# Kernel tuning notes

Hardware: AMD Instinct MI355X
Metric: run time of the kernel (lower is better)

Reference implementation:

```python
import jax, jax.numpy as jnp
import numpy as np

KERNEL_SIZE = 32
STRIDE = 16
SELECT_SIZE = 64
TOP_N = 16
NUM_INIT = 1      # slc_att_num_init_blocks
NUM_LOCAL = 2     # slc_att_num_local_blocks
NHEADS = 32
NKV = 8
KEEP = 999999.0   # keep_prob_value


def setup_inputs() -> dict:
    key = jax.random.key(0)
    ks = jax.random.split(key, 4)
    b, m, n, d = 1, 2048, 2048, 128
    C = (n - KERNEL_SIZE) // STRIDE + 1  # 127 compressed blocks
    q = jax.random.normal(ks[0], (b, m, NHEADS, d), jnp.float32)
    k = jax.random.normal(ks[1], (b, n, NKV, d), jnp.float32)
    v = jax.random.normal(ks[2], (b, n, NKV, d), jnp.float32)
    p = jax.random.uniform(ks[3], (b, NHEADS, m, C), jnp.float32)
    return {"q": q, "k": k, "v": v, "p": p}


def _select_indices(p, n):
    """NSA-style compressed-block -> select-block scoring + causal top-k."""
    S = -(-n // SELECT_SIZE)            # num select blocks
    C = p.shape[-1]
    cs = jnp.arange(C) * STRIDE                       # compress starts
    ss = jnp.arange(S) * SELECT_SIZE                  # select starts
    se = jnp.minimum(ss + SELECT_SIZE, n)             # select ends
    # overlap area between compress window c and select block s, /stride
    area = jnp.clip(jnp.minimum(cs[None, :] + KERNEL_SIZE, se[:, None])
                    - jnp.maximum(cs[None, :], ss[:, None]), 0)
    W = area.astype(jnp.float32) / STRIDE             # [S, C]
    sp = jnp.einsum('bhmc,sc->bhms', p.astype(jnp.float32), W)  # [b,qh,m,S]
    b, qh, m, _ = p.shape
    g = qh // NKV
    sp = sp.reshape(b, NKV, g, m, S).max(axis=2)      # agg_type='max' -> [b,kh,m,S]
    row = jnp.arange(m)
    rb = row // SELECT_SIZE                           # row's own block idx
    # init block (NUM_INIT==1 -> block 0 for every row, torch broadcast semantics)
    sp = sp.at[:, :, :, 0].set(KEEP)
    # local blocks
    for l in range(NUM_LOCAL):
        sp = sp.at[:, :, row, jnp.maximum(rb - l, 0)].set(KEEP)
    K = min(S, TOP_N)
    _, idx = jax.lax.top_k(sp, K)                     # [b,kh,m,K]
    # causal clamp: at most rb+1 blocks per row; rest -> sentinel S
    clip = jnp.arange(K)[None, :] >= (rb + 1)[:, None]   # [m,K]
    idx = jnp.where(clip[None, None], S, idx)
    return idx, S


def reference(q, k, v, p):
    b, m, qh, d = q.shape
    n, kh = k.shape[1], k.shape[2]
    g = qh // kh
    idx, S = _select_indices(jax.lax.stop_gradient(p), n)   # selection is inference_mode
    qt = q.transpose(0, 2, 1, 3)                            # [b,qh,m,d]
    kt = jnp.repeat(k.transpose(0, 2, 1, 3), g, axis=1)     # repeat_kv -> [b,qh,n,d]
    vt = jnp.repeat(v.transpose(0, 2, 1, 3), g, axis=1)
    scale = d ** -0.5
    s = jnp.einsum('bhmd,bhnd->bhmn', qt, kt) * scale       # dense score matrix
    idx_full = jnp.repeat(idx, g, axis=1)                   # [b,qh,m,K]
    # scatter selected block ids into membership mask over S+1 slots (S = sentinel)
    blk_mask = (idx_full[..., None] == jnp.arange(S + 1)).any(axis=-2)  # [b,qh,m,S+1]
    key_block = jnp.arange(n) // SELECT_SIZE
    key_mask = blk_mask[:, :, :, key_block]                 # expand blocks -> keys
    causal = jnp.tril(jnp.ones((m, n), bool))
    mask = key_mask & causal
    s = jnp.where(mask, s, -jnp.inf)
    attn = jax.nn.softmax(s.astype(jnp.float32), axis=-1).astype(q.dtype)
    o = jnp.einsum('bhmn,bhnd->bhmd', attn, vt)
    return o.transpose(0, 2, 1, 3)                          # [b,m,qh,d]
```

## Files before the change

### kernel.cpp

```cpp
#include <hip/hip_runtime.h>

typedef __bf16 bf16x8 __attribute__((ext_vector_type(8)));
typedef float f32x4 __attribute__((ext_vector_type(4)));
typedef float f32x16 __attribute__((ext_vector_type(16)));

__device__ __forceinline__ unsigned short f2bf(float x) {
  union { float f; unsigned u; } a; a.f = x;
  unsigned r = a.u + 0x7FFFu + ((a.u >> 16) & 1u);
  return (unsigned short)(r >> 16);
}

__device__ __forceinline__ float exp2f_fast(float x) {
  return __builtin_amdgcn_exp2f(x);
}

__device__ __forceinline__ unsigned cvtpk_bf16(float lo, float hi) {
  unsigned r;
  asm("v_cvt_pk_bf16_f32 %0, %1, %2" : "=v"(r) : "v"(lo), "v"(hi));
  return r;
}

__device__ __forceinline__ int swap23(int x) {
  return (x & ~12) | ((x & 4) << 1) | ((x & 8) >> 1);
}

__global__ __launch_bounds__(256) void prep_kernel(const float* __restrict__ k,
                                                   const float* __restrict__ v,
                                                   const float* __restrict__ p,
                                                   unsigned short* __restrict__ Kt,
                                                   unsigned short* __restrict__ Vt,
                                                   unsigned* __restrict__ sm) {
  const int bx = blockIdx.x;
  if (bx < 4096) {
    const int wid = bx * 4 + (threadIdx.x >> 6);
    const int lane = threadIdx.x & 63;
    const int kv = wid >> 11;
    const int m = wid & 2047;
    const int rb = m >> 6;
    const int s = lane & 31;
    const int c0 = 4 * s - 1;
    float best = -1.f;
    for (int g = 0; g < 2; ++g) {
      int h = kv * 4 + (lane >> 5) * 2 + g;
      const float* pr = p + ((size_t)h * 2048 + m) * 127;
      float acc = 0.f;
      if (c0 >= 0) acc = fmaf(pr[c0], 1.f, acc);
      acc = fmaf(pr[c0 + 1], 2.f, acc);
      acc = fmaf(pr[c0 + 2], 2.f, acc);
      acc = fmaf(pr[c0 + 3], 2.f, acc);
      if (c0 + 4 < 127) acc = fmaf(pr[c0 + 4], 1.f, acc);
      best = fmaxf(best, acc);
    }
    best = fmaxf(best, __shfl_xor(best, 32));
    const int rbm1 = rb > 0 ? rb - 1 : 0;
    if (s == 0 || s == rb || s == rbm1) best = 999999.0f;
    const int half = lane & 32;
    int cnt = 0;
#pragma unroll
    for (int o = 1; o <= 16; ++o) {
      int oo = half ? (o + 16) : o;
      int os = (s + oo) & 31;
      float ov = __shfl(best, half | os);
      bool gr = (ov > best) || (ov == best && os < s);
      cnt += (gr && oo < 32) ? 1 : 0;
    }
    int rank = cnt + __shfl_xor(cnt, 32);
    const int kmax = min(rb + 1, 16);
    unsigned long long bal = __ballot(rank < kmax);
    if (lane == 0) sm[(size_t)kv * 2048 + m] = (unsigned)(bal & 0xffffffffu);
  } else if (bx < 4352) {
    const int kvs = bx - 4096;
    const int kv = kvs >> 5, s = kvs & 31;
    const int lane = threadIdx.x & 63;
    const int jg = threadIdx.x >> 6;
    const int c = lane & 31, hb = lane >> 5;
    const int posl = swap23(c);
    unsigned short* dst = Kt + ((size_t)kvs << 13);
#pragma unroll
    for (int jj = 0; jj < 4; ++jj) {
      int j = jg * 4 + jj;
      int pos = s * 64 + ((j >> 3) << 5) + posl;
      int d0 = ((j & 7) << 4) + (hb << 3);
      const float* src = k + (((size_t)pos * 8 + kv) << 7) + d0;
      float4 a = *(const float4*)src;
      float4 b = *(const float4*)(src + 4);
      union { bf16x8 w; unsigned short u[8]; } t;
      t.u[0] = f2bf(a.x); t.u[1] = f2bf(a.y); t.u[2] = f2bf(a.z); t.u[3] = f2bf(a.w);
      t.u[4] = f2bf(b.x); t.u[5] = f2bf(b.y); t.u[6] = f2bf(b.z); t.u[7] = f2bf(b.w);
      *(bf16x8*)(dst + ((j * 64 + lane) << 3)) = t.w;
    }
  } else {
    const int kvs = bx - 4352;
    const int kv = kvs >> 5, s = kvs & 31;
    const int lane = threadIdx.x & 63;
    const int jg = threadIdx.x >> 6;
    const int c = lane & 31, hb = lane >> 5;
    unsigned short* dst = Vt + ((size_t)kvs << 13);
#pragma unroll
    for (int jj = 0; jj < 4; ++jj) {
      int j = jg * 4 + jj;
      int db = j >> 2, kk = j & 3;
      int d = (db << 5) + c;
      int pos0 = s * 64 + (kk << 4) + (hb << 3);
      union { bf16x8 w; unsigned short u[8]; } t;
#pragma unroll
      for (int i = 0; i < 8; ++i)
        t.u[i] = f2bf(v[(((size_t)(pos0 + i) * 8 + kv) << 7) + d]);
      *(bf16x8*)(dst + ((j * 64 + lane) << 3)) = t.w;
    }
  }
}

__global__ __launch_bounds__(256, 2) void attn_kernel(
    const unsigned short* __restrict__ Kt,
    const unsigned short* __restrict__ Vt,
    const float* __restrict__ q,
    const unsigned* __restrict__ sm,
    float* __restrict__ out) {
  const int wg = blockIdx.x;
  const int kv = wg & 7;
  const int zi = wg >> 3;
  const int z = (zi < 32) ? (2 * zi + 1) : (126 - 2 * zi);
  const int m0 = z * 32;
  const int rb = z >> 1;
  const int tid = threadIdx.x;
  const int w = tid >> 6, lane = tid & 63;
  const int c = lane & 31, hb = lane >> 5;
  const int row = m0 + w * 8 + (c & 7);
  const int head = kv * 4 + (c >> 3);

  const float qs = 0.08838834764831845f * 1.4426950408889634f;
  bf16x8 qf[8];
  {
    const float* qp = q + ((size_t)row * 32 + head) * 128 + hb * 8;
#pragma unroll
    for (int ks = 0; ks < 8; ++ks) {
      float4 a = *(const float4*)(qp + ks * 16);
      float4 b = *(const float4*)(qp + ks * 16 + 4);
      union { bf16x8 v; unsigned w4[4]; } t;
      t.w4[0] = cvtpk_bf16(a.x * qs, a.y * qs);
      t.w4[1] = cvtpk_bf16(a.z * qs, a.w * qs);
      t.w4[2] = cvtpk_bf16(b.x * qs, b.y * qs);
      t.w4[3] = cvtpk_bf16(b.z * qs, b.w * qs);
      qf[ks] = t.v;
    }
  }
  const unsigned selr = sm[(size_t)kv * 2048 + row];
  unsigned aW = selr;
  aW |= __shfl_xor(aW, 1);
  aW |= __shfl_xor(aW, 2);
  aW |= __shfl_xor(aW, 4);
  aW &= (2u << rb) - 1u;

  f32x16 oacc[4];
#pragma unroll
  for (int i = 0; i < 4; ++i)
#pragma unroll
    for (int e = 0; e < 16; ++e) oacc[i][e] = 0.f;
  float lrun = 0.f;

  const unsigned short* Kb = Kt + ((size_t)(kv * 32) << 13);
  const unsigned short* Vb = Vt + ((size_t)(kv * 32) << 13);

  unsigned bits = aW;
  while (bits) {
    const int s = __builtin_ctz(bits);
    bits &= bits - 1;
    const unsigned short* kt = Kb + ((size_t)s << 13);
    const unsigned short* vt = Vb + ((size_t)s << 13);
    bf16x8 kf[16];
#pragma unroll
    for (int j = 0; j < 16; ++j)
      kf[j] = *(const bf16x8*)(kt + ((j * 64 + lane) << 3));
    f32x16 a0 = {}, a1 = {};
#pragma unroll
    for (int ks = 0; ks < 8; ++ks)
      a0 = __builtin_amdgcn_mfma_f32_32x32x16_bf16(kf[ks], qf[ks], a0, 0, 0, 0);
#pragma unroll
    for (int ks = 0; ks < 8; ++ks)
      a1 = __builtin_amdgcn_mfma_f32_32x32x16_bf16(kf[8 + ks], qf[ks], a1, 0, 0, 0);
    bf16x8 vf[16];
#pragma unroll
    for (int j = 0; j < 16; ++j)
      vf[j] = *(const bf16x8*)(vt + ((j * 64 + lane) << 3));
    int lim = ((selr >> s) & 1u) ? ((s == rb) ? (row & 63) : 63) : -1;
    int limadj = lim - 8 * hb;
    float pv[32];
#pragma unroll
    for (int j = 0; j < 32; ++j) {
      int P0 = ((j >> 4) << 5) + (((j >> 3) & 1) << 4) + (j & 7);
      float x = (j < 16) ? a0[j & 15] : a1[j & 15];
      pv[j] = exp2f_fast((P0 <= limadj) ? x : -3.0e38f);
    }
    float s0[8];
#pragma unroll
    for (int j = 0; j < 8; ++j)
      s0[j] = (pv[4 * j] + pv[4 * j + 1]) + (pv[4 * j + 2] + pv[4 * j + 3]);
    float psum = ((s0[0] + s0[1]) + (s0[2] + s0[3])) + ((s0[4] + s0[5]) + (s0[6] + s0[7]));
    psum += __shfl_xor(psum, 32);
    lrun += psum;
    bf16x8 pf[4];
#pragma unroll
    for (int kk = 0; kk < 4; ++kk) {
      union { bf16x8 v; unsigned w4[4]; } t;
      t.w4[0] = cvtpk_bf16(pv[8 * kk + 0], pv[8 * kk + 1]);
      t.w4[1] = cvtpk_bf16(pv[8 * kk + 2], pv[8 * kk + 3]);
      t.w4[2] = cvtpk_bf16(pv[8 * kk + 4], pv[8 * kk + 5]);
      t.w4[3] = cvtpk_bf16(pv[8 * kk + 6], pv[8 * kk + 7]);
      pf[kk] = t.v;
    }
#pragma unroll
    for (int jp = 0; jp < 16; ++jp)
      oacc[jp >> 2] = __builtin_amdgcn_mfma_f32_32x32x16_bf16(vf[jp], pf[jp & 3], oacc[jp >> 2], 0, 0, 0);
  }
  const float inv = 1.f / lrun;
  float* op = out + ((size_t)row * 32 + head) * 128;
#pragma unroll
  for (int db = 0; db < 4; ++db) {
#pragma unroll
    for (int rg = 0; rg < 4; ++rg) {
      float4 o4;
      o4.x = oacc[db][4 * rg + 0] * inv;
      o4.y = oacc[db][4 * rg + 1] * inv;
      o4.z = oacc[db][4 * rg + 2] * inv;
      o4.w = oacc[db][4 * rg + 3] * inv;
      *(float4*)&op[db * 32 + rg * 8 + hb * 4] = o4;
    }
  }
}

extern "C" void kernel_launch(void* const* d_in, const int* in_sizes, int n_in,
                              void* d_out, int out_size, void* d_ws, size_t ws_size,
                              hipStream_t stream) {
  const float* q = (const float*)d_in[0];
  const float* k = (const float*)d_in[1];
  const float* v = (const float*)d_in[2];
  const float* p = (const float*)d_in[3];
  float* out = (float*)d_out;
  unsigned short* Kt = (unsigned short*)d_ws;
  unsigned short* Vt = (unsigned short*)((char*)d_ws + (size_t)4 * 1024 * 1024);
  unsigned* sm = (unsigned*)((char*)d_ws + (size_t)8 * 1024 * 1024);

  prep_kernel<<<4608, 256, 0, stream>>>(k, v, p, Kt, Vt, sm);
  attn_kernel<<<512, 256, 0, stream>>>(Kt, Vt, q, sm, out);
}
```

Before: 70.78 us.

## Double-buffer K/V blocks in LDS via async global-to-LDS loads shared across waves

Changes the attention loop so the workgroup iterates over the union of all waves' selected blocks. Each block's K/V tiles are staged cooperatively into double-buffered shared memory using global_load_lds, and the next block is prefetched while the current one is computed. This replaces per-wave redundant global loads with one shared load per workgroup and overlaps memory latency with MFMA work. In exchange it adds barriers per block, forces every wave to step through blocks it may not need, and uses 64KB of LDS, which may limit occupancy at two workgroups per CU.

```diff
diff --git a/kernel.cpp b/kernel.cpp
--- a/kernel.cpp
+++ b/kernel.cpp
@@ -18,6 +18,12 @@
   unsigned r;
   asm("v_cvt_pk_bf16_f32 %0, %1, %2" : "=v"(r) : "v"(lo), "v"(hi));
   return r;
+}
+
+__device__ __forceinline__ void gl_lds16(const void* g, void* l) {
+  __builtin_amdgcn_global_load_lds(
+      (const __attribute__((address_space(1))) void*)g,
+      (__attribute__((address_space(3))) void*)l, 16, 0, 0);
 }
 
 __device__ __forceinline__ int swap23(int x) {
@@ -129,6 +135,10 @@
   const int row = m0 + w * 8 + (c & 7);
   const int head = kv * 4 + (c >> 3);
 
+  __shared__ unsigned short Kl[2][8192];
+  __shared__ unsigned short Vl[2][8192];
+  __shared__ unsigned Ush;
+
   const float qs = 0.08838834764831845f * 1.4426950408889634f;
   bf16x8 qf[8];
   {
@@ -150,7 +160,30 @@
   aW |= __shfl_xor(aW, 1);
   aW |= __shfl_xor(aW, 2);
   aW |= __shfl_xor(aW, 4);
-  aW &= (2u << rb) - 1u;
+  const unsigned cmask = (2u << rb) - 1u;
+  aW &= cmask;
+  if (tid == 0) Ush = 0;
+  __syncthreads();
+  if (lane == 0) atomicOr(&Ush, aW);
+  __syncthreads();
+  const unsigned U = Ush;
+
+  const unsigned short* KtKv = Kt + ((size_t)(kv * 32) << 13);
+  const unsigned short* VtKv = Vt + ((size_t)(kv * 32) << 13);
+
+  auto STAGE = [&](int b, int si) {
+    const size_t so = (size_t)si << 13;
+#pragma unroll
+    for (int jj = 0; jj < 4; ++jj) {
+      int j = w * 4 + jj;
+      gl_lds16(KtKv + so + (j << 9) + (lane << 3), &Kl[b][j << 9]);
+    }
+#pragma unroll
+    for (int jj = 0; jj < 4; ++jj) {
+      int j = w * 4 + jj;
+      gl_lds16(VtKv + so + (j << 9) + (lane << 3), &Vl[b][j << 9]);
+    }
+  };
 
   f32x16 oacc[4];
 #pragma unroll
@@ -159,59 +192,75 @@
     for (int e = 0; e < 16; ++e) oacc[i][e] = 0.f;
   float lrun = 0.f;
 
-  const unsigned short* Kb = Kt + ((size_t)(kv * 32) << 13);
-  const unsigned short* Vb = Vt + ((size_t)(kv * 32) << 13);
-
-  unsigned bits = aW;
-  while (bits) {
-    const int s = __builtin_ctz(bits);
-    bits &= bits - 1;
-    const unsigned short* kt = Kb + ((size_t)s << 13);
-    const unsigned short* vt = Vb + ((size_t)s << 13);
-    bf16x8 kf[16];
-#pragma unroll
-    for (int j = 0; j < 16; ++j)
-      kf[j] = *(const bf16x8*)(kt + ((j * 64 + lane) << 3));
-    f32x16 a0 = {}, a1 = {};
-#pragma unroll
-    for (int ks = 0; ks < 8; ++ks)
-      a0 = __builtin_amdgcn_mfma_f32_32x32x16_bf16(kf[ks], qf[ks], a0, 0, 0, 0);
-#pragma unroll
-    for (int ks = 0; ks < 8; ++ks)
-      a1 = __builtin_amdgcn_mfma_f32_32x32x16_bf16(kf[8 + ks], qf[ks], a1, 0, 0, 0);
-    bf16x8 vf[16];
-#pragma unroll
-    for (int j = 0; j < 16; ++j)
-      vf[j] = *(const bf16x8*)(vt + ((j * 64 + lane) << 3));
-    int lim = ((selr >> s) & 1u) ? ((s == rb) ? (row & 63) : 63) : -1;
-    int limadj = lim - 8 * hb;
-    float pv[32];
-#pragma unroll
-    for (int j = 0; j < 32; ++j) {
-      int P0 = ((j >> 4) << 5) + (((j >> 3) & 1) << 4) + (j & 7);
-      float x = (j < 16) ? a0[j & 15] : a1[j & 15];
-      pv[j] = exp2f_fast((P0 <= limadj) ? x : -3.0e38f);
-    }
-    float s0[8];
-#pragma unroll
-    for (int j = 0; j < 8; ++j)
-      s0[j] = (pv[4 * j] + pv[4 * j + 1]) + (pv[4 * j + 2] + pv[4 * j + 3]);
-    float psum = ((s0[0] + s0[1]) + (s0[2] + s0[3])) + ((s0[4] + s0[5]) + (s0[6] + s0[7]));
-    psum += __shfl_xor(psum, 32);
-    lrun += psum;
-    bf16x8 pf[4];
-#pragma unroll
-    for (int kk = 0; kk < 4; ++kk) {
-      union { bf16x8 v; unsigned w4[4]; } t;
-      t.w4[0] = cvtpk_bf16(pv[8 * kk + 0], pv[8 * kk + 1]);
-      t.w4[1] = cvtpk_bf16(pv[8 * kk + 2], pv[8 * kk + 3]);
-      t.w4[2] = cvtpk_bf16(pv[8 * kk + 4], pv[8 * kk + 5]);
-      t.w4[3] = cvtpk_bf16(pv[8 * kk + 6], pv[8 * kk + 7]);
-      pf[kk] = t.v;
-    }
-#pragma unroll
-    for (int jp = 0; jp < 16; ++jp)
-      oacc[jp >> 2] = __builtin_amdgcn_mfma_f32_32x32x16_bf16(vf[jp], pf[jp & 3], oacc[jp >> 2], 0, 0, 0);
+  int s = 0;
+  int cur = 0;
+  STAGE(0, 0);
+  while (s >= 0) {
+    int ns = -1;
+    if (s < 31) {
+      unsigned rest = U >> (s + 1);
+      if (rest) ns = s + 1 + __builtin_ctz(rest);
+    }
+    if (ns >= 0) {
+      STAGE(cur ^ 1, ns);
+      asm volatile("s_waitcnt vmcnt(8)" ::: "memory");
+    } else {
+      asm volatile("s_waitcnt vmcnt(0)" ::: "memory");
+    }
+    __builtin_amdgcn_s_barrier();
+    asm volatile("" ::: "memory");
+    if ((aW >> s) & 1u) {
+      const unsigned short* KL = &Kl[cur][0];
+      const unsigned short* VL = &Vl[cur][0];
+      bf16x8 kf[16];
+#pragma unroll
+      for (int j = 0; j < 16; ++j)
+        kf[j] = *(const bf16x8*)&KL[(j << 9) + (lane << 3)];
+      f32x16 a0 = {}, a1 = {};
+#pragma unroll
+      for (int ks = 0; ks < 8; ++ks)
+        a0 = __builtin_amdgcn_mfma_f32_32x32x16_bf16(kf[ks], qf[ks], a0, 0, 0, 0);
+#pragma unroll
+      for (int ks = 0; ks < 8; ++ks)
+        a1 = __builtin_amdgcn_mfma_f32_32x32x16_bf16(kf[8 + ks], qf[ks], a1, 0, 0, 0);
+      bf16x8 vf[16];
+#pragma unroll
+      for (int j = 0; j < 16; ++j)
+        vf[j] = *(const bf16x8*)&VL[(j << 9) + (lane << 3)];
+      int lim = ((selr >> s) & 1u) ? ((s == rb) ? (row & 63) : 63) : -1;
+      int limadj = lim - 8 * hb;
+      float pv[32];
+#pragma unroll
+      for (int j = 0; j < 32; ++j) {
+        int P0 = ((j >> 4) << 5) + (((j >> 3) & 1) << 4) + (j & 7);
+        float x = (j < 16) ? a0[j & 15] : a1[j & 15];
+        pv[j] = exp2f_fast((P0 <= limadj) ? x : -3.0e38f);
+      }
+      float s0[8];
+#pragma unroll
+      for (int j = 0; j < 8; ++j)
+        s0[j] = (pv[4 * j] + pv[4 * j + 1]) + (pv[4 * j + 2] + pv[4 * j + 3]);
+      float psum = ((s0[0] + s0[1]) + (s0[2] + s0[3])) + ((s0[4] + s0[5]) + (s0[6] + s0[7]));
+      psum += __shfl_xor(psum, 32);
+      lrun += psum;
+      bf16x8 pf[4];
+#pragma unroll
+      for (int kk = 0; kk < 4; ++kk) {
+        union { bf16x8 v; unsigned w4[4]; } t;
+        t.w4[0] = cvtpk_bf16(pv[8 * kk + 0], pv[8 * kk + 1]);
+        t.w4[1] = cvtpk_bf16(pv[8 * kk + 2], pv[8 * kk + 3]);
+        t.w4[2] = cvtpk_bf16(pv[8 * kk + 4], pv[8 * kk + 5]);
+        t.w4[3] = cvtpk_bf16(pv[8 * kk + 6], pv[8 * kk + 7]);
+        pf[kk] = t.v;
+      }
+#pragma unroll
+      for (int jp = 0; jp < 16; ++jp)
+        oacc[jp >> 2] = __builtin_amdgcn_mfma_f32_32x32x16_bf16(vf[jp], pf[jp & 3], oacc[jp >> 2], 0, 0, 0);
+    }
+    asm volatile("" ::: "memory");
+    __builtin_amdgcn_s_barrier();
+    cur ^= 1;
+    s = ns;
   }
   const float inv = 1.f / lrun;
   float* op = out + ((size_t)row * 32 + head) * 128;
```

After: 75.67 us. 1.07x slower.
